# Performance work log

Measured on AMD Instinct MI355X. Metric: run time of the kernel, lower is better.

The kernel has to match this reference:

```python
import jax, jax.numpy as jnp
import numpy as np

N_ENTITIES = 100000
EMBED = 64
BATCH = 4096
TEMPERATURE = 0.2


def _infonce(v1, v2, temperature):
    # v1, v2: [B, d]
    B = v1.shape[0]
    sim11 = v1 @ v1.T  # [B,B]
    sim22 = v2 @ v2.T
    sim12 = v1 @ v2.T
    eye = jnp.eye(B, dtype=bool)
    neg_inf = jnp.float32(-jnp.inf)
    sim11 = jnp.where(eye, neg_inf, sim11)
    sim22 = jnp.where(eye, neg_inf, sim22)
    logits1 = jnp.concatenate([sim12, sim11], axis=-1)          # [B,2B]
    logits2 = jnp.concatenate([sim22, sim12.T], axis=-1)        # [B,2B]
    logits = jnp.concatenate([logits1, logits2], axis=0) / temperature  # [2B,2B]
    targets = jnp.arange(2 * B)
    logp = jax.nn.log_softmax(logits, axis=-1)
    return -jnp.mean(jnp.take_along_axis(logp, targets[:, None], axis=-1))


def setup_inputs() -> dict:
    key = jax.random.key(0)
    k1, k2, k3, k4, k5, k6 = jax.random.split(key, 6)
    return {
        "input_u_list": jax.random.randint(k1, (BATCH,), 0, N_ENTITIES),
        "input_i_list": jax.random.randint(k2, (BATCH,), 0, N_ENTITIES),
        "u_sub1_embeddings": jax.random.normal(k3, (N_ENTITIES, EMBED), dtype=jnp.float32),
        "i_sub1_embeddings": jax.random.normal(k4, (N_ENTITIES, EMBED), dtype=jnp.float32),
        "u_sub2_embeddings": jax.random.normal(k5, (N_ENTITIES, EMBED), dtype=jnp.float32),
        "i_sub2_embeddings": jax.random.normal(k6, (N_ENTITIES, EMBED), dtype=jnp.float32),
    }


def reference(input_u_list, input_i_list, u_sub1_embeddings, i_sub1_embeddings,
              u_sub2_embeddings, i_sub2_embeddings):
    # user branch: gather + L2-normalize
    u1 = u_sub1_embeddings[input_u_list]
    u2 = u_sub2_embeddings[input_u_list]
    u1 = u1 / jnp.linalg.norm(u1, axis=1, keepdims=True)
    u2 = u2 / jnp.linalg.norm(u2, axis=1, keepdims=True)
    user_cl_loss = _infonce(u1, u2, TEMPERATURE)
    # item branch: gather only (the original does NOT normalize items)
    i1 = i_sub1_embeddings[input_i_list]
    i2 = i_sub2_embeddings[input_i_list]
    item_cl_loss = _infonce(i1, i2, TEMPERATURE)
    return user_cl_loss + item_cl_loss
```

## Files before the change

kernel.cpp:

```cpp
#include <hip/hip_runtime.h>
#include <hip/hip_bf16.h>
#include <math.h>

#define B_SZ   4096
#define D      64
#define RPB    8192
#define NCHUNK 6
#define NPART  16
#define LN2    0.69314718055994531f
#define PRESCALE 2.6857914f
#define DEFER_THR 60.0f

typedef __attribute__((ext_vector_type(8))) short  bf16x8;
typedef __attribute__((ext_vector_type(4))) float  f32x4;

__device__ __forceinline__ float fexp2(float x) { return __builtin_amdgcn_exp2f(x); }

typedef const __attribute__((address_space(1))) unsigned int* gptr_t;
typedef __attribute__((address_space(3))) unsigned int* lptr_t;
__device__ __forceinline__ void stage16(const void* g, void* l) {
    __builtin_amdgcn_global_load_lds((gptr_t)g, (lptr_t)l, 16, 0, 0);
}


__global__ __launch_bounds__(256) void gather_kernel(
    const int* __restrict__ u_idx, const int* __restrict__ i_idx,
    const float* __restrict__ u1e, const float* __restrict__ i1e,
    const float* __restrict__ u2e, const float* __restrict__ i2e,
    __hip_bfloat16* __restrict__ Xbf, float* __restrict__ dots,
    float* __restrict__ out)
{
    const int tid  = threadIdx.x;
    if (blockIdx.x == 0 && tid == 0) *out = 0.f;
    const int wave = tid >> 6, lane = tid & 63;
    const int g      = blockIdx.x * 4 + wave;
    const int branch = g >> 12;
    const int i      = g & (B_SZ - 1);
    const int idx    = (branch == 0) ? u_idx[i] : i_idx[i];
    const float* s1  = (branch == 0) ? u1e : i1e;
    const float* s2  = (branch == 0) ? u2e : i2e;

    float v1 = s1[(size_t)idx * D + lane];
    float v2 = s2[(size_t)idx * D + lane];
    if (branch == 0) {
        float a = v1 * v1, b = v2 * v2;
        #pragma unroll
        for (int o = 32; o > 0; o >>= 1) {
            a += __shfl_xor(a, o, 64);
            b += __shfl_xor(b, o, 64);
        }
        v1 *= rsqrtf(a);
        v2 *= rsqrtf(b);
    }
    float p = v1 * v2;
    #pragma unroll
    for (int o = 32; o > 0; o >>= 1) p += __shfl_xor(p, o, 64);
    if (lane == 0) dots[g] = p;

    const size_t row1 = (size_t)branch * RPB + i;
    Xbf[row1 * D + lane]          = __float2bfloat16(v1 * PRESCALE);
    Xbf[(row1 + B_SZ) * D + lane] = __float2bfloat16(v2 * PRESCALE);
}

template<int IS_USER>
__device__ __forceinline__ void gram_body(
    const __hip_bfloat16* __restrict__ Xb, float2* __restrict__ P,
    const int bx, const int chunk, char* sm)
{
    const int tid  = threadIdx.x;
    const int r0   = bx * 128;
    const int wave = tid >> 6, lane = tid & 63;
    const int wm = wave >> 1, wn = wave & 1;
    const int quad = lane >> 4, tx = lane & 15;

    const int cstart = chunk * 11 - (chunk > 4 ? chunk - 4 : 0);
    const int ntile  = (chunk < 4) ? 11 : 10;

    const int srow_b = wave * 32 + (lane >> 3);
    const int scb    = ((lane & 7) * 16) ^ ((lane >> 3) << 4);
    const char* Xbytes = (const char*)Xb;

    {
        const char* src = Xbytes + (size_t)cstart * 16384;
        #pragma unroll
        for (int k = 0; k < 4; ++k)
            stage16(src + (srow_b + k * 8) * 128 + scb,
                    sm + wave * 4096 + k * 1024);
    }

    bf16x8 afr[4][2];
    const __hip_bfloat16* Ap = Xb + (size_t)(r0 + wm * 64 + tx) * D + quad * 8;
    #pragma unroll
    for (int mt = 0; mt < 4; ++mt)
        #pragma unroll
        for (int ks = 0; ks < 2; ++ks)
            afr[mt][ks] = *(const bf16x8*)(Ap + mt * 16 * D + ks * 32);

    float m_run[16], s_run[16];
    #pragma unroll
    for (int r = 0; r < 16; ++r) { m_run[r] = -INFINITY; s_run[r] = 0.f; }

    const int lrq  = wm * 64 + quad * 4;
    const int lcol = wn * 64 + tx;

    const int rbase = (wn * 64 + tx) * 128;
    const int key   = (tx & 7) << 4;
    const int cb0   = (quad * 16) ^ key;
    const int cb1   = (64 + quad * 16) ^ key;

    __syncthreads();

    #pragma unroll 1
    for (int t = 0; t < ntile; ++t) {
        const int ct  = cstart + t;
        const int cur = (t & 1) << 14;

        if (t + 1 < ntile) {
            const char* src = Xbytes + (size_t)(ct + 1) * 16384;
            char* dst = sm + (((t + 1) & 1) << 14) + wave * 4096;
            #pragma unroll
            for (int k = 0; k < 4; ++k)
                stage16(src + (srow_b + k * 8) * 128 + scb, dst + k * 1024);
        }

        bf16x8 b0[4], b1[4];
        #pragma unroll
        for (int nt = 0; nt < 4; ++nt) {
            b0[nt] = *(const bf16x8*)(sm + cur + rbase + nt * 2048 + cb0);
            b1[nt] = *(const bf16x8*)(sm + cur + rbase + nt * 2048 + cb1);
        }

        f32x4 acc[4][4];
        const f32x4 z = {0.f, 0.f, 0.f, 0.f};
        #pragma unroll
        for (int nt = 0; nt < 4; ++nt)
            #pragma unroll
            for (int mt = 0; mt < 4; ++mt)
                acc[mt][nt] = __builtin_amdgcn_mfma_f32_16x16x32_bf16(afr[mt][0], b0[nt], z, 0, 0, 0);
        #pragma unroll
        for (int nt = 0; nt < 4; ++nt)
            #pragma unroll
            for (int mt = 0; mt < 4; ++mt)
                acc[mt][nt] = __builtin_amdgcn_mfma_f32_16x16x32_bf16(afr[mt][1], b1[nt], acc[mt][nt], 0, 0, 0);

        const bool diag = (ct == bx);
        #pragma unroll
        for (int mt = 0; mt < 4; ++mt) {
            #pragma unroll
            for (int rr = 0; rr < 4; ++rr) {
                float y0 = acc[mt][0][rr], y1 = acc[mt][1][rr],
                      y2 = acc[mt][2][rr], y3 = acc[mt][3][rr];
                if (diag) {
                    const int dr = lrq + mt * 16 + rr - lcol;
                    if (dr == 0)  y0 = -INFINITY;
                    if (dr == 16) y1 = -INFINITY;
                    if (dr == 32) y2 = -INFINITY;
                    if (dr == 48) y3 = -INFINITY;
                }
                const int r = mt * 4 + rr;
                if (IS_USER) {
                    s_run[r] += fexp2(y0) + fexp2(y1) + fexp2(y2) + fexp2(y3);
                } else {
                    float mx = fmaxf(fmaxf(y0, y1), fmaxf(y2, y3));
                    if (__builtin_expect(mx > m_run[r] + DEFER_THR, 0)) {
                        s_run[r] *= fexp2(m_run[r] - mx);
                        m_run[r] = mx;
                    }
                    const float m = m_run[r];
                    s_run[r] += fexp2(y0 - m) + fexp2(y1 - m)
                              + fexp2(y2 - m) + fexp2(y3 - m);
                }
            }
        }

        __syncthreads();
    }

    #pragma unroll
    for (int r = 0; r < 16; ++r) {
        float m = IS_USER ? 0.f : m_run[r];
        float s = s_run[r];
        #pragma unroll
        for (int o = 1; o < 16; o <<= 1) {
            if (IS_USER) {
                s += __shfl_xor(s, o, 64);
            } else {
                float om = __shfl_xor(m, o, 64);
                float os = __shfl_xor(s, o, 64);
                float M  = fmaxf(m, om);
                s = s * fexp2(m - M) + os * fexp2(om - M);
                m = M;
            }
        }
        if (tx == 0) {
            const int grow = r0 + wm * 64 + (r >> 2) * 16 + quad * 4 + (r & 3);
            P[(size_t)grow * NPART + chunk * 2 + wn] = make_float2(m, s);
        }
    }
}

__global__ __launch_bounds__(256, 3) void gram_lse_fused(
    const __hip_bfloat16* __restrict__ Xb0, float2* __restrict__ P0)
{
    __shared__ __align__(16) char sm[32768];
    const int bid    = blockIdx.x;
    const int branch = bid & 1;
    const int rest   = bid >> 1;
    const int bx     = rest & 63;
    const int chunk  = rest >> 6;
    const __hip_bfloat16* Xb = Xb0 + (size_t)branch * RPB * D;
    float2* P = P0 + (size_t)branch * RPB * NPART;
    if (branch == 0) gram_body<1>(Xb, P, bx, chunk, sm);
    else             gram_body<0>(Xb, P, bx, chunk, sm);
}

__global__ __launch_bounds__(256) void merge_kernel(
    const float2* __restrict__ P, const float* __restrict__ dots,
    float* __restrict__ out)
{
    __shared__ float red[4];
    const int tid  = threadIdx.x;
    const int wave = tid >> 6, lane = tid & 63;

    float vsum = 0.f;
    #pragma unroll
    for (int k = 0; k < 8; ++k) {
        const int vb  = blockIdx.x * 8 + k;
        const int gw  = vb * 4 + wave;
        const int row = gw * 4 + (lane >> 4);
        const int c   = lane & 15;

        float2 p = (c < 12) ? P[(size_t)row * NPART + c] : make_float2(0.f, 0.f);
        float m = p.x, s = p.y;
        #pragma unroll
        for (int o = 1; o < 16; o <<= 1) {
            float om = __shfl_xor(m, o, 64);
            float os = __shfl_xor(s, o, 64);
            float M  = fmaxf(m, om);
            s = s * fexp2(m - M) + os * fexp2(om - M);
            m = M;
        }

        if ((lane & 15) == 0)
            vsum += LN2 * (m + log2f(s)) * (1.0f / (float)RPB);
        if (tid < 8)
            vsum -= dots[vb * 8 + tid] * (5.0f / (float)B_SZ);
    }

    float v = vsum;
    #pragma unroll
    for (int o = 32; o > 0; o >>= 1) v += __shfl_xor(v, o, 64);
    if (lane == 0) red[wave] = v;
    __syncthreads();
    if (tid == 0)
        atomicAdd(out, red[0] + red[1] + red[2] + red[3]);
}

extern "C" void kernel_launch(void* const* d_in, const int* in_sizes, int n_in,
                              void* d_out, int out_size, void* d_ws, size_t ws_size,
                              hipStream_t stream) {
    const int*   u_idx = (const int*)d_in[0];
    const int*   i_idx = (const int*)d_in[1];
    const float* u1e   = (const float*)d_in[2];
    const float* i1e   = (const float*)d_in[3];
    const float* u2e   = (const float*)d_in[4];
    const float* i2e   = (const float*)d_in[5];
    float* out = (float*)d_out;

    __hip_bfloat16* Xbf = (__hip_bfloat16*)d_ws;
    float*  dots = (float*)((char*)d_ws + 2 * RPB * D * 2);
    float2* P    = (float2*)((char*)dots + RPB * sizeof(float));

    gather_kernel<<<dim3(2048), dim3(256), 0, stream>>>(
        u_idx, i_idx, u1e, i1e, u2e, i2e, Xbf, dots, out);
    gram_lse_fused<<<dim3(768), dim3(256), 0, stream>>>(Xbf, P);
    merge_kernel<<<dim3(128), dim3(256), 0, stream>>>(P, dots, out);
}
```

Baseline: 171.5 us.

## Restructure gram kernel into single-wave blocks with 64-row tiles and 8 column chunks

Replaces the 256-thread, 4-wave blocks (128x128 tiles, 6 uneven column chunks, block-wide barriers) with one-wave 64-thread blocks that each own 64 rows and 16 column tiles of 64, launching 2048 blocks. Removing __syncthreads and giving each wave its own double-buffered LDS is meant to cut barrier stalls and raise scheduling flexibility, with a sched_barrier placed so the next tile's prefetch is issued after the current LDS reads. The merge kernel is adjusted to 8 partials per row. The cost is that each B tile is staged by one wave instead of shared across four, which increases global/L2 traffic, and the single-wave buffer reuse relies on in-order issue without explicit waits.

```diff
diff --git a/kernel.cpp b/kernel.cpp
--- a/kernel.cpp
+++ b/kernel.cpp
@@ -5,8 +5,9 @@
 #define B_SZ   4096
 #define D      64
 #define RPB    8192
-#define NCHUNK 6
-#define NPART  16
+#define NCHUNK 8
+#define TPW    16
+#define NPART  8
 #define LN2    0.69314718055994531f
 #define PRESCALE 2.6857914f
 #define DEFER_THR 60.0f
@@ -65,31 +66,25 @@
 template<int IS_USER>
 __device__ __forceinline__ void gram_body(
     const __hip_bfloat16* __restrict__ Xb, float2* __restrict__ P,
-    const int bx, const int chunk, char* sm)
-{
-    const int tid  = threadIdx.x;
-    const int r0   = bx * 128;
-    const int wave = tid >> 6, lane = tid & 63;
-    const int wm = wave >> 1, wn = wave & 1;
+    const int rowg, const int chunk, char* sm)
+{
+    const int lane = threadIdx.x & 63;
     const int quad = lane >> 4, tx = lane & 15;
-
-    const int cstart = chunk * 11 - (chunk > 4 ? chunk - 4 : 0);
-    const int ntile  = (chunk < 4) ? 11 : 10;
-
-    const int srow_b = wave * 32 + (lane >> 3);
+    const int r0   = rowg * 64;
+
+    const int srow_b = lane >> 3;
     const int scb    = ((lane & 7) * 16) ^ ((lane >> 3) << 4);
     const char* Xbytes = (const char*)Xb;
 
     {
-        const char* src = Xbytes + (size_t)cstart * 16384;
-        #pragma unroll
-        for (int k = 0; k < 4; ++k)
-            stage16(src + (srow_b + k * 8) * 128 + scb,
-                    sm + wave * 4096 + k * 1024);
+        const char* src = Xbytes + (size_t)(chunk * TPW) * 8192;
+        #pragma unroll
+        for (int k = 0; k < 8; ++k)
+            stage16(src + (srow_b + k * 8) * 128 + scb, sm + k * 1024 + lane * 16);
     }
 
     bf16x8 afr[4][2];
-    const __hip_bfloat16* Ap = Xb + (size_t)(r0 + wm * 64 + tx) * D + quad * 8;
+    const __hip_bfloat16* Ap = Xb + (size_t)(r0 + tx) * D + quad * 8;
     #pragma unroll
     for (int mt = 0; mt < 4; ++mt)
         #pragma unroll
@@ -100,28 +95,17 @@
     #pragma unroll
     for (int r = 0; r < 16; ++r) { m_run[r] = -INFINITY; s_run[r] = 0.f; }
 
-    const int lrq  = wm * 64 + quad * 4;
-    const int lcol = wn * 64 + tx;
-
-    const int rbase = (wn * 64 + tx) * 128;
+    const int lrq = quad * 4;
+
+    const int rbase = tx * 128;
     const int key   = (tx & 7) << 4;
     const int cb0   = (quad * 16) ^ key;
     const int cb1   = (64 + quad * 16) ^ key;
 
-    __syncthreads();
-
     #pragma unroll 1
-    for (int t = 0; t < ntile; ++t) {
-        const int ct  = cstart + t;
-        const int cur = (t & 1) << 14;
-
-        if (t + 1 < ntile) {
-            const char* src = Xbytes + (size_t)(ct + 1) * 16384;
-            char* dst = sm + (((t + 1) & 1) << 14) + wave * 4096;
-            #pragma unroll
-            for (int k = 0; k < 4; ++k)
-                stage16(src + (srow_b + k * 8) * 128 + scb, dst + k * 1024);
-        }
+    for (int t = 0; t < TPW; ++t) {
+        const int ct  = chunk * TPW + t;
+        const int cur = (t & 1) << 13;
 
         bf16x8 b0[4], b1[4];
         #pragma unroll
@@ -129,6 +113,15 @@
             b0[nt] = *(const bf16x8*)(sm + cur + rbase + nt * 2048 + cb0);
             b1[nt] = *(const bf16x8*)(sm + cur + rbase + nt * 2048 + cb1);
         }
+        __builtin_amdgcn_sched_barrier(0);
+
+        if (t + 1 < TPW) {
+            const char* src = Xbytes + (size_t)(ct + 1) * 8192;
+            char* dst = sm + (((t + 1) & 1) << 13);
+            #pragma unroll
+            for (int k = 0; k < 8; ++k)
+                stage16(src + (srow_b + k * 8) * 128 + scb, dst + k * 1024 + lane * 16);
+        }
 
         f32x4 acc[4][4];
         const f32x4 z = {0.f, 0.f, 0.f, 0.f};
@@ -143,7 +136,7 @@
             for (int mt = 0; mt < 4; ++mt)
                 acc[mt][nt] = __builtin_amdgcn_mfma_f32_16x16x32_bf16(afr[mt][1], b1[nt], acc[mt][nt], 0, 0, 0);
 
-        const bool diag = (ct == bx);
+        const bool diag = (ct == rowg);
         #pragma unroll
         for (int mt = 0; mt < 4; ++mt) {
             #pragma unroll
@@ -151,7 +144,7 @@
                 float y0 = acc[mt][0][rr], y1 = acc[mt][1][rr],
                       y2 = acc[mt][2][rr], y3 = acc[mt][3][rr];
                 if (diag) {
-                    const int dr = lrq + mt * 16 + rr - lcol;
+                    const int dr = lrq + mt * 16 + rr - tx;
                     if (dr == 0)  y0 = -INFINITY;
                     if (dr == 16) y1 = -INFINITY;
                     if (dr == 32) y2 = -INFINITY;
@@ -172,8 +165,6 @@
                 }
             }
         }
-
-        __syncthreads();
     }
 
     #pragma unroll
@@ -193,25 +184,25 @@
             }
         }
         if (tx == 0) {
-            const int grow = r0 + wm * 64 + (r >> 2) * 16 + quad * 4 + (r & 3);
-            P[(size_t)grow * NPART + chunk * 2 + wn] = make_float2(m, s);
-        }
-    }
-}
-
-__global__ __launch_bounds__(256, 3) void gram_lse_fused(
+            const int grow = r0 + (r >> 2) * 16 + quad * 4 + (r & 3);
+            P[(size_t)grow * NPART + chunk] = make_float2(m, s);
+        }
+    }
+}
+
+__global__ __launch_bounds__(64) void gram_lse_fused(
     const __hip_bfloat16* __restrict__ Xb0, float2* __restrict__ P0)
 {
-    __shared__ __align__(16) char sm[32768];
+    __shared__ __align__(16) char sm[16384];
     const int bid    = blockIdx.x;
     const int branch = bid & 1;
     const int rest   = bid >> 1;
-    const int bx     = rest & 63;
-    const int chunk  = rest >> 6;
+    const int rowg   = rest & 127;
+    const int chunk  = rest >> 7;
     const __hip_bfloat16* Xb = Xb0 + (size_t)branch * RPB * D;
     float2* P = P0 + (size_t)branch * RPB * NPART;
-    if (branch == 0) gram_body<1>(Xb, P, bx, chunk, sm);
-    else             gram_body<0>(Xb, P, bx, chunk, sm);
+    if (branch == 0) gram_body<1>(Xb, P, rowg, chunk, sm);
+    else             gram_body<0>(Xb, P, rowg, chunk, sm);
 }
 
 __global__ __launch_bounds__(256) void merge_kernel(
@@ -224,16 +215,14 @@
 
     float vsum = 0.f;
     #pragma unroll
-    for (int k = 0; k < 8; ++k) {
-        const int vb  = blockIdx.x * 8 + k;
-        const int gw  = vb * 4 + wave;
-        const int row = gw * 4 + (lane >> 4);
-        const int c   = lane & 15;
-
-        float2 p = (c < 12) ? P[(size_t)row * NPART + c] : make_float2(0.f, 0.f);
+    for (int it = 0; it < 4; ++it) {
+        const int row = blockIdx.x * 128 + it * 32 + wave * 8 + (lane >> 3);
+        const int c   = lane & 7;
+
+        float2 p = P[(size_t)row * NPART + c];
         float m = p.x, s = p.y;
         #pragma unroll
-        for (int o = 1; o < 16; o <<= 1) {
+        for (int o = 1; o < 8; o <<= 1) {
             float om = __shfl_xor(m, o, 64);
             float os = __shfl_xor(s, o, 64);
             float M  = fmaxf(m, om);
@@ -241,11 +230,12 @@
             m = M;
         }
 
-        if ((lane & 15) == 0)
+        if ((lane & 7) == 0)
             vsum += LN2 * (m + log2f(s)) * (1.0f / (float)RPB);
-        if (tid < 8)
-            vsum -= dots[vb * 8 + tid] * (5.0f / (float)B_SZ);
-    }
+    }
+
+    if (tid < 64)
+        vsum -= dots[blockIdx.x * 64 + tid] * (5.0f / (float)B_SZ);
 
     float v = vsum;
     #pragma unroll
@@ -273,6 +263,6 @@
 
     gather_kernel<<<dim3(2048), dim3(256), 0, stream>>>(
         u_idx, i_idx, u1e, i1e, u2e, i2e, Xbf, dots, out);
-    gram_lse_fused<<<dim3(768), dim3(256), 0, stream>>>(Xbf, P);
+    gram_lse_fused<<<dim3(2048), dim3(64), 0, stream>>>(Xbf, P);
     merge_kernel<<<dim3(128), dim3(256), 0, stream>>>(P, dots, out);
 }
```

New measurement: 186.6 us. 1.09x slower.
